# Optimization experiments

Hardware: AMD Instinct MI355X
Metric: run time of the kernel (lower is better)

## Reference

```python
import jax, jax.numpy as jnp
import numpy as np

NUM_HEADS = 32


def setup_inputs() -> dict:
    key = jax.random.key(0)
    ks = jax.random.split(key, 6)
    B, S, E = 1, 2048, 2560
    return {
        "hidden_states": jax.random.normal(ks[0], (B, S, E), dtype=jnp.float32),
        "attention_mask": jnp.zeros((B, 1, 1, S), dtype=jnp.float32),
        "position_bias": jax.random.normal(ks[1], (NUM_HEADS, S, S), dtype=jnp.float32),
        "c_attn_w": jax.random.normal(ks[2], (E, 3 * E), dtype=jnp.float32) * 0.02,
        "c_attn_b": jax.random.normal(ks[3], (3 * E,), dtype=jnp.float32) * 0.02,
        "c_proj_w": jax.random.normal(ks[4], (E, E), dtype=jnp.float32) * 0.02,
        "c_proj_b": jax.random.normal(ks[5], (E,), dtype=jnp.float32) * 0.02,
    }


def reference(hidden_states, attention_mask, position_bias, c_attn_w, c_attn_b, c_proj_w, c_proj_b):
    B, S, E = hidden_states.shape
    H = NUM_HEADS
    D = E // H  # head_dim = 80

    # Fused QKV projection (GPT2-style Conv1D: x @ W + b)
    qkv = hidden_states @ c_attn_w + c_attn_b            # [B, S, 3E]
    q, k, v = jnp.split(qkv, 3, axis=-1)

    def split_heads(t):
        return t.reshape(B, S, H, D).transpose(0, 2, 1, 3)  # [B, H, S, D]

    q, k, v = split_heads(q), split_heads(k), split_heads(v)

    # muP scaling: attn_scale_power=1.0 -> divide by head_dim (not sqrt)
    scores = jnp.einsum("bhqd,bhkd->bhqk", q, k) / jnp.asarray(D, q.dtype)
    scores = scores + attention_mask                     # additive mask [B,1,1,S]
    scores = scores + position_bias[None]                # ALiBi bias [1,H,S,S]

    attn = jax.nn.softmax(scores, axis=-1)               # dropout p=0 -> identity
    out = jnp.einsum("bhqk,bhkd->bhqd", attn, v)         # [B, H, S, D]
    out = out.transpose(0, 2, 1, 3).reshape(B, S, E)     # merge heads

    out = out @ c_proj_w + c_proj_b                      # output projection
    return out
```

## Files before the change

### kernel.cpp

```cpp
#include <hip/hip_runtime.h>
#include <stdint.h>

#define S_LEN 2048
#define EMB   2560
#define NH    32
#define HD    80
#define DP    96

typedef __bf16 bf16x8 __attribute__((ext_vector_type(8)));
typedef float  f32x4  __attribute__((ext_vector_type(4)));

__device__ __forceinline__ ushort f2bf(float x) {
    union { float f; uint32_t u; } v; v.f = x;
    return (ushort)((v.u + 0x7FFFu + ((v.u >> 16) & 1u)) >> 16);
}

__device__ __forceinline__ bf16x8 ldg8(const ushort* p) {
    return *reinterpret_cast<const bf16x8*>(p);
}

__device__ __forceinline__ void gload_lds16(const void* g, void* l) {
    __builtin_amdgcn_global_load_lds((__attribute__((address_space(1))) void*)g,
                                     (__attribute__((address_space(3))) void*)l,
                                     16, 0, 0);
}

__global__ void cvt_f32_bf16(const float* __restrict__ in, ushort* __restrict__ out, int n4) {
    int i = blockIdx.x * blockDim.x + threadIdx.x;
    if (i >= n4) return;
    float4 v = reinterpret_cast<const float4*>(in)[i];
    ushort4 r;
    r.x = f2bf(v.x); r.y = f2bf(v.y); r.z = f2bf(v.z); r.w = f2bf(v.w);
    reinterpret_cast<ushort4*>(out)[i] = r;
}

__global__ void pad_zero(ushort* __restrict__ Qb, ushort* __restrict__ Kb) {
    int i   = blockIdx.x * blockDim.x + threadIdx.x;
    int row = i & 65535;
    ushort* base = ((i >> 16) ? Kb : Qb) + (size_t)row * DP + HD;
    uint4 z = {0, 0, 0, 0};
    *reinterpret_cast<uint4*>(base)     = z;
    *reinterpret_cast<uint4*>(base + 8) = z;
}

__global__ void transpose_cvt(const float* __restrict__ in, ushort* __restrict__ out, int R, int C) {
    __shared__ float tile[32][33];
    const int bx = blockIdx.x << 5;
    const int by = blockIdx.y << 5;
    const int tx = threadIdx.x, ty = threadIdx.y;
#pragma unroll
    for (int i = 0; i < 4; ++i)
        tile[ty + 8 * i][tx] = in[(size_t)(by + ty + 8 * i) * C + bx + tx];
    __syncthreads();
#pragma unroll
    for (int i = 0; i < 4; ++i)
        out[(size_t)(bx + ty + 8 * i) * R + by + tx] = f2bf(tile[tx][ty + 8 * i]);
}

template <int EPI>
__global__ __launch_bounds__(256)
void gemm_bt(const ushort* __restrict__ A, const ushort* __restrict__ BT,
             int M, int N, int Kd, const float* __restrict__ bvec,
             ushort* __restrict__ Qo, ushort* __restrict__ Ko, ushort* __restrict__ Vo,
             float* __restrict__ Co)
{
    __shared__ ushort As[128 * 64];
    __shared__ ushort Bs[128 * 64];

    const int nbn = N >> 7;
    const int nwg = gridDim.x;
    const int cpx = nwg >> 3;
    const int bid = blockIdx.x;
    const int wg  = (bid & 7) * cpx + (bid >> 3);
    const int bm  = wg / nbn;
    const int bn  = wg - bm * nbn;

    const int tid  = threadIdx.x;
    const int w    = tid >> 6, lane = tid & 63;
    const int lo   = lane & 15, hi = lane >> 4;
    const int wr   = w >> 1, wc = w & 1;

    const int srow  = tid >> 3;
    const int sbyte = (tid & 7) << 4;

    f32x4 acc[4][4] = {};

    const char* aG = (const char*)(A  + (size_t)bm * 128 * Kd);
    const char* bG = (const char*)(BT + (size_t)bn * 128 * Kd);
    const size_t rowBytes = (size_t)Kd * 2;

    for (int k0 = 0; k0 < Kd; k0 += 64) {
        __syncthreads();
#pragma unroll
        for (int is = 0; is < 4; ++is) {
            int r  = (is << 5) + srow;
            int sw = sbyte ^ ((r & 7) << 4);
            const char* ga = aG + (size_t)r * rowBytes + (size_t)k0 * 2 + sw;
            const char* gb = bG + (size_t)r * rowBytes + (size_t)k0 * 2 + sw;
            char* la = (char*)As + (is << 12) + (w << 10);
            char* lb = (char*)Bs + (is << 12) + (w << 10);
            gload_lds16(ga, la);
            gload_lds16(gb, lb);
        }
        asm volatile("s_waitcnt vmcnt(0)" ::: "memory");
        __syncthreads();
#pragma unroll
        for (int kk = 0; kk < 2; ++kk) {
            bf16x8 af[4], bf[4];
#pragma unroll
            for (int m = 0; m < 4; ++m) {
                int r   = (wr << 6) + (m << 4) + lo;
                int off = (r << 7) + ((((kk << 6) + (hi << 4))) ^ ((r & 7) << 4));
                af[m] = *(const bf16x8*)((const char*)As + off);
            }
#pragma unroll
            for (int n = 0; n < 4; ++n) {
                int r   = (wc << 6) + (n << 4) + lo;
                int off = (r << 7) + ((((kk << 6) + (hi << 4))) ^ ((r & 7) << 4));
                bf[n] = *(const bf16x8*)((const char*)Bs + off);
            }
#pragma unroll
            for (int m = 0; m < 4; ++m)
#pragma unroll
                for (int n = 0; n < 4; ++n)
                    acc[m][n] = __builtin_amdgcn_mfma_f32_16x16x32_bf16(af[m], bf[n], acc[m][n], 0, 0, 0);
        }
    }

    const int gr_base = bm * 128 + (wr << 6);
    const int gc_base = bn * 128 + (wc << 6);
#pragma unroll
    for (int m = 0; m < 4; ++m) {
        int gr0 = gr_base + (m << 4) + (hi << 2);
#pragma unroll
        for (int n = 0; n < 4; ++n) {
            int gc = gc_base + (n << 4) + lo;
            float bv = bvec[gc];
            if (EPI == 0) {
                int sec = gc / EMB;
                int rr  = gc - sec * EMB;
                int h   = rr / HD;
                int d   = rr - h * HD;
                if (sec == 2) {
                    ushort4 pk;
                    pk.x = f2bf(acc[m][n][0] + bv);
                    pk.y = f2bf(acc[m][n][1] + bv);
                    pk.z = f2bf(acc[m][n][2] + bv);
                    pk.w = f2bf(acc[m][n][3] + bv);
                    *reinterpret_cast<ushort4*>(Vo + ((size_t)h * HD + d) * S_LEN + gr0) = pk;
                } else {
#pragma unroll
                    for (int j = 0; j < 4; ++j) {
                        float vv = acc[m][n][j] + bv;
                        int s = gr0 + j;
                        if (sec == 0) Qo[((size_t)h * S_LEN + s) * DP + d] = f2bf(vv * (1.0f / 80.0f));
                        else          Ko[((size_t)h * S_LEN + s) * DP + d] = f2bf(vv);
                    }
                }
            } else {
#pragma unroll
                for (int j = 0; j < 4; ++j)
                    Co[(size_t)(gr0 + j) * N + gc] = acc[m][n][j] + bv;
            }
        }
    }
}

__global__ __launch_bounds__(512, 4)
void attn_fwd(const ushort* __restrict__ Q, const ushort* __restrict__ K,
              const ushort* __restrict__ VT, const float* __restrict__ bias,
              const float* __restrict__ mask, ushort* __restrict__ ctx)
{
    __shared__ ushort Ks[2][64 * 96];
    __shared__ ushort Vs[2][80 * 64];
    __shared__ ushort P[8][16][72];

    const int bid = blockIdx.x;
    const int l_  = (bid & 7) * 64 + (bid >> 3);
    const int h   = l_ >> 4;
    const int qb  = (l_ & 15) << 7;
    const int tid = threadIdx.x;
    const int w   = tid >> 6, lane = tid & 63;
    const int lo  = lane & 15, hi = lane >> 4;
    const int qrow = qb + (w << 4);

    const ushort* qp = Q + ((size_t)(h * S_LEN + qrow + lo)) * DP + hi * 8;
    bf16x8 qf0 = ldg8(qp), qf1 = ldg8(qp + 32), qf2 = ldg8(qp + 64);

    const char*  kg = (const char*)(K + (size_t)h * S_LEN * DP);
    const char*  vg = (const char*)(VT + (size_t)h * HD * S_LEN);
    const float* bb = bias + (size_t)(h * S_LEN + qrow + hi * 4) * S_LEN + lo;

    int offK0, offK1;
    {
        int b0 = (w << 10) + lane * 16;
        int r0 = b0 / 192, y0 = b0 - r0 * 192;
        offK0 = r0 * 192 + (y0 ^ ((y0 < 128 ? (r0 & 7) : (r0 & 3)) << 4));
        int b1 = ((w + 8) << 10) + lane * 16;
        int r1 = b1 / 192, y1 = b1 - r1 * 192;
        offK1 = r1 * 192 + (y1 ^ ((y1 < 128 ? (r1 & 7) : (r1 & 3)) << 4));
    }

    f32x4 o[5] = {};
    float l_p[4] = {0.f, 0.f, 0.f, 0.f};
    float m_r[4] = {-1e30f, -1e30f, -1e30f, -1e30f};
    float bc[4][4], bn[4][4], mn_[4];

    auto stage_k = [&](int buf, int kt) {
        const char* src = kg + (size_t)kt * 192;
        gload_lds16(src + offK0, (char*)Ks[buf] + (w << 10));
        if (w < 4)
            gload_lds16(src + offK1, (char*)Ks[buf] + ((w + 8) << 10));
    };
    auto stage_v = [&](int buf, int kt) {
        int r0 = (w << 3) + (lane >> 3);
        int s0 = ((lane & 7) << 4) ^ ((r0 & 7) << 4);
        gload_lds16(vg + (size_t)r0 * (S_LEN * 2) + (size_t)kt * 2 + s0,
                    (char*)Vs[buf] + (w << 10));
        if (w < 2) {
            int r1 = ((w + 8) << 3) + (lane >> 3);
            int s1 = ((lane & 7) << 4) ^ ((r1 & 7) << 4);
            gload_lds16(vg + (size_t)r1 * (S_LEN * 2) + (size_t)kt * 2 + s1,
                        (char*)Vs[buf] + ((w + 8) << 10));
        }
    };
    auto bload = [&](int kt) {
#pragma unroll
        for (int n = 0; n < 4; ++n) {
            mn_[n] = mask[kt + n * 16 + lo];
#pragma unroll
            for (int j = 0; j < 4; ++j)
                bn[n][j] = __builtin_nontemporal_load(bb + (size_t)j * S_LEN + kt + n * 16);
        }
    };
    auto rotate = [&]() {
#pragma unroll
        for (int n = 0; n < 4; ++n)
#pragma unroll
            for (int j = 0; j < 4; ++j)
                bc[n][j] = bn[n][j] + mn_[n];
    };

    stage_k(0, 0); stage_v(0, 0); bload(0); rotate();
    __syncthreads();

#pragma unroll 1
    for (int t = 0; t < 32; ++t) {
        const int kt = t << 6;
        const int cb = t & 1;
        if (t < 31) { stage_k(cb ^ 1, kt + 64); stage_v(cb ^ 1, kt + 64); bload(kt + 64); }

        const char* tb = (const char*)Ks[cb];
        f32x4 sc[4] = {};
        __builtin_amdgcn_s_setprio(1);
#pragma unroll
        for (int n = 0; n < 4; ++n) {
            const int r  = (n << 4) + lo;
            const char* rp = tb + r * 192;
            const int s7 = (r & 7) << 4, s3 = (r & 3) << 4;
            sc[n] = __builtin_amdgcn_mfma_f32_16x16x32_bf16(qf0, *(const bf16x8*)(rp + ((hi * 16) ^ s7)),        sc[n], 0, 0, 0);
            sc[n] = __builtin_amdgcn_mfma_f32_16x16x32_bf16(qf1, *(const bf16x8*)(rp + ((64 + hi * 16) ^ s7)),   sc[n], 0, 0, 0);
            sc[n] = __builtin_amdgcn_mfma_f32_16x16x32_bf16(qf2, *(const bf16x8*)(rp + ((128 + hi * 16) ^ s3)),  sc[n], 0, 0, 0);
        }
        __builtin_amdgcn_s_setprio(0);

#pragma unroll
        for (int n = 0; n < 4; ++n)
#pragma unroll
            for (int j = 0; j < 4; ++j)
                sc[n][j] += bc[n][j];

        float tm[4];
#pragma unroll
        for (int j = 0; j < 4; ++j)
            tm[j] = fmaxf(fmaxf(sc[0][j], sc[1][j]), fmaxf(sc[2][j], sc[3][j]));
#pragma unroll
        for (int off = 1; off <= 8; off <<= 1)
#pragma unroll
            for (int j = 0; j < 4; ++j)
                tm[j] = fmaxf(tm[j], __shfl_xor(tm[j], off, 64));

        float al[4];
#pragma unroll
        for (int j = 0; j < 4; ++j) {
            float mnew = fmaxf(m_r[j], tm[j]);
            al[j] = __builtin_amdgcn_exp2f((m_r[j] - mnew) * 1.44269504f);
            m_r[j] = mnew;
            l_p[j] *= al[j];
        }
#pragma unroll
        for (int dn = 0; dn < 5; ++dn)
#pragma unroll
            for (int j = 0; j < 4; ++j)
                o[dn][j] *= al[j];
#pragma unroll
        for (int n = 0; n < 4; ++n)
#pragma unroll
            for (int j = 0; j < 4; ++j) {
                float p = __builtin_amdgcn_exp2f((sc[n][j] - m_r[j]) * 1.44269504f);
                l_p[j] += p;
                P[w][hi * 4 + j][n * 16 + lo] = f2bf(p);
            }
        asm volatile("s_waitcnt lgkmcnt(0)" ::: "memory");
        __builtin_amdgcn_sched_barrier(0);
        bf16x8 pf0 = ldg8(&P[w][lo][hi * 8]);
        bf16x8 pf1 = ldg8(&P[w][lo][32 + hi * 8]);

        const char* vb_ = (const char*)Vs[cb];
        __builtin_amdgcn_s_setprio(1);
#pragma unroll
        for (int dn = 0; dn < 5; ++dn) {
            const int rv = (dn << 4) + lo;
            const char* vp = vb_ + (rv << 7);
            const int sv = (rv & 7) << 4;
            o[dn] = __builtin_amdgcn_mfma_f32_16x16x32_bf16(pf0, *(const bf16x8*)(vp + ((hi * 16) ^ sv)),      o[dn], 0, 0, 0);
            o[dn] = __builtin_amdgcn_mfma_f32_16x16x32_bf16(pf1, *(const bf16x8*)(vp + ((64 + hi * 16) ^ sv)), o[dn], 0, 0, 0);
        }
        __builtin_amdgcn_s_setprio(0);

        rotate();
        __syncthreads();
    }

    float inv[4];
#pragma unroll
    for (int j = 0; j < 4; ++j) {
        float t = l_p[j];
        t += __shfl_xor(t, 1, 64); t += __shfl_xor(t, 2, 64);
        t += __shfl_xor(t, 4, 64); t += __shfl_xor(t, 8, 64);
        inv[j] = 1.0f / t;
    }
    ushort* cp = ctx + (size_t)(qrow + hi * 4) * EMB + h * HD + lo;
#pragma unroll
    for (int dn = 0; dn < 5; ++dn)
#pragma unroll
        for (int j = 0; j < 4; ++j)
            cp[(size_t)j * EMB + dn * 16] = f2bf(o[dn][j] * inv[j]);
}

extern "C" void kernel_launch(void* const* d_in, const int* in_sizes, int n_in,
                              void* d_out, int out_size, void* d_ws, size_t ws_size,
                              hipStream_t stream)
{
    const float* hs     = (const float*)d_in[0];
    const float* mask   = (const float*)d_in[1];
    const float* pbias  = (const float*)d_in[2];
    const float* attn_w = (const float*)d_in[3];
    const float* attn_b = (const float*)d_in[4];
    const float* proj_w = (const float*)d_in[5];
    const float* proj_b = (const float*)d_in[6];
    float* outp = (float*)d_out;

    char* ws = (char*)d_ws;
    ushort* hsB    = (ushort*)(ws);
    ushort* attnWT = (ushort*)(ws + 10485760ull);
    ushort* Qb     = (ushort*)(ws + 49807360ull);
    ushort* Kb     = (ushort*)(ws + 62390272ull);
    ushort* VTb    = (ushort*)(ws + 74973184ull);
    ushort* ctx    = hsB;
    ushort* projWT = attnWT;

    cvt_f32_bf16<<<5120, 256, 0, stream>>>(hs, hsB, 1310720);
    transpose_cvt<<<dim3(7680 / 32, 2560 / 32), dim3(32, 8), 0, stream>>>(attn_w, attnWT, 2560, 7680);
    pad_zero<<<512, 256, 0, stream>>>(Qb, Kb);

    gemm_bt<0><<<960, 256, 0, stream>>>(hsB, attnWT, 2048, 7680, 2560, attn_b,
                                        Qb, Kb, VTb, nullptr);

    attn_fwd<<<512, 512, 0, stream>>>(Qb, Kb, VTb, pbias, mask, ctx);

    transpose_cvt<<<dim3(2560 / 32, 2560 / 32), dim3(32, 8), 0, stream>>>(proj_w, projWT, 2560, 2560);

    gemm_bt<1><<<320, 256, 0, stream>>>(ctx, projWT, 2048, 2560, 2560, proj_b,
                                        nullptr, nullptr, nullptr, outp);
}
```

Baseline: 371.2 us.

## Add 8-wave 128x256 QKV GEMM with triple-buffered direct-to-LDS pipeline

Replaces the generic QKV projection GEMM with a dedicated 512-thread kernel using 128x256 tiles, a three-stage LDS ring filled by global_load_lds with XOR swizzling, and interleaved LDS reads, prefetches and MFMA phases under setprio. The aim is to hide global load latency and raise MFMA utilisation for the largest GEMM. The old template keeps only the output-projection epilogue. The cost is 144 KB of LDS per block, which limits residency to one block per CU, and a hand-scheduled pipeline that is sensitive to the placement of its waitcnt and barrier instructions.

```diff
diff --git a/kernel.cpp b/kernel.cpp
--- a/kernel.cpp
+++ b/kernel.cpp
@@ -55,6 +55,157 @@
 #pragma unroll
     for (int i = 0; i < 4; ++i)
         out[(size_t)(bx + ty + 8 * i) * R + by + tx] = f2bf(tile[tx][ty + 8 * i]);
+}
+
+#define MF(a, b, c) __builtin_amdgcn_mfma_f32_16x16x32_bf16((a), (b), (c), 0, 0, 0)
+
+#define STAGE(kt2, j) do {                                                          \
+    char* _d = Lds + ((kt2) % 3) * 49152 + ldsW[(j)];                               \
+    if ((j) < 2) gload_lds16(aG + (size_t)(kt2) * 128 + srcA[(j)], _d);             \
+    else         gload_lds16(bG + (size_t)(kt2) * 128 + srcB[(j) - 2], _d);         \
+} while (0)
+
+#define LDA(mi, kk) (*(const bf16x8*)(sbase + ((wr * 64 + (mi) * 16 + lo) * 128 +   \
+                      ((((kk) * 64) + hi * 16) ^ ((lo & 7) << 4)))))
+#define LDB(ni, kk) (*(const bf16x8*)(sbase + 16384 +                               \
+                      ((wc * 64 + (ni) * 16 + lo) * 128 +                           \
+                      ((((kk) * 64) + hi * 16) ^ ((lo & 7) << 4)))))
+
+__global__ __launch_bounds__(512)
+void gemm8p_qkv(const ushort* __restrict__ A, const ushort* __restrict__ BT,
+                const float* __restrict__ bvec,
+                ushort* __restrict__ Qo, ushort* __restrict__ Ko, ushort* __restrict__ Vo)
+{
+    __shared__ char Lds[3 * 49152];
+
+    const int NT  = 40;
+    const int nbn = 30;
+    const int bid = blockIdx.x;
+    const int wg  = (bid & 7) * 60 + (bid >> 3);
+    const int bm  = wg / nbn, bn = wg - bm * nbn;
+
+    const int tid = threadIdx.x, w = tid >> 6, lane = tid & 63;
+    const int lo  = lane & 15, hi = lane >> 4;
+    const int wr  = w >> 2, wc = w & 3;
+
+    const char* aG = (const char*)(A  + (size_t)bm * 128 * 2560);
+    const char* bG = (const char*)(BT + (size_t)bn * 256 * 2560);
+
+    int srcA[2], srcB[4], ldsW[6];
+#pragma unroll
+    for (int j = 0; j < 6; ++j) {
+        int Lb = j * 8192 + w * 1024 + lane * 16;
+        ldsW[j] = j * 8192 + w * 1024;
+        int y = Lb & 127;
+        if (j < 2) {
+            int r = Lb >> 7;
+            srcA[j] = r * 5120 + (y ^ ((r & 7) << 4));
+        } else {
+            int r = (Lb - 16384) >> 7;
+            srcB[j - 2] = r * 5120 + (y ^ ((r & 7) << 4));
+        }
+    }
+
+    f32x4  acc[4][4] = {};
+    bf16x8 Afr[2][2], Bfr[4][2];
+
+#pragma unroll
+    for (int j = 0; j < 6; ++j) STAGE(0, j);
+#pragma unroll
+    for (int j = 0; j < 6; ++j) STAGE(1, j);
+
+#pragma unroll 1
+    for (int t = 0; t < NT; ++t) {
+        const char* sbase = Lds + (t % 3) * 49152;
+        const int  t2 = t + 2;
+        const bool pf = (t2 < NT);
+
+        if (t < NT - 1) asm volatile("s_waitcnt vmcnt(6)" ::: "memory");
+        else            asm volatile("s_waitcnt vmcnt(0)" ::: "memory");
+        __builtin_amdgcn_s_barrier();
+
+        Afr[0][0] = LDA(0, 0); Afr[0][1] = LDA(0, 1);
+        Afr[1][0] = LDA(1, 0); Afr[1][1] = LDA(1, 1);
+        Bfr[0][0] = LDB(0, 0); Bfr[0][1] = LDB(0, 1);
+        Bfr[1][0] = LDB(1, 0); Bfr[1][1] = LDB(1, 1);
+        if (pf) { STAGE(t2, 0); STAGE(t2, 1); }
+        __builtin_amdgcn_s_barrier();
+        asm volatile("s_waitcnt lgkmcnt(0)" ::: "memory");
+        __builtin_amdgcn_sched_barrier(0);
+        __builtin_amdgcn_s_setprio(1);
+        acc[0][0] = MF(Afr[0][0], Bfr[0][0], acc[0][0]); acc[0][0] = MF(Afr[0][1], Bfr[0][1], acc[0][0]);
+        acc[0][1] = MF(Afr[0][0], Bfr[1][0], acc[0][1]); acc[0][1] = MF(Afr[0][1], Bfr[1][1], acc[0][1]);
+        acc[1][0] = MF(Afr[1][0], Bfr[0][0], acc[1][0]); acc[1][0] = MF(Afr[1][1], Bfr[0][1], acc[1][0]);
+        acc[1][1] = MF(Afr[1][0], Bfr[1][0], acc[1][1]); acc[1][1] = MF(Afr[1][1], Bfr[1][1], acc[1][1]);
+        __builtin_amdgcn_s_setprio(0);
+
+        Bfr[2][0] = LDB(2, 0); Bfr[2][1] = LDB(2, 1);
+        Bfr[3][0] = LDB(3, 0); Bfr[3][1] = LDB(3, 1);
+        if (pf) { STAGE(t2, 2); STAGE(t2, 3); }
+        __builtin_amdgcn_s_barrier();
+        asm volatile("s_waitcnt lgkmcnt(0)" ::: "memory");
+        __builtin_amdgcn_sched_barrier(0);
+        __builtin_amdgcn_s_setprio(1);
+        acc[0][2] = MF(Afr[0][0], Bfr[2][0], acc[0][2]); acc[0][2] = MF(Afr[0][1], Bfr[2][1], acc[0][2]);
+        acc[0][3] = MF(Afr[0][0], Bfr[3][0], acc[0][3]); acc[0][3] = MF(Afr[0][1], Bfr[3][1], acc[0][3]);
+        acc[1][2] = MF(Afr[1][0], Bfr[2][0], acc[1][2]); acc[1][2] = MF(Afr[1][1], Bfr[2][1], acc[1][2]);
+        acc[1][3] = MF(Afr[1][0], Bfr[3][0], acc[1][3]); acc[1][3] = MF(Afr[1][1], Bfr[3][1], acc[1][3]);
+        __builtin_amdgcn_s_setprio(0);
+
+        Afr[0][0] = LDA(2, 0); Afr[0][1] = LDA(2, 1);
+        Afr[1][0] = LDA(3, 0); Afr[1][1] = LDA(3, 1);
+        if (pf) STAGE(t2, 4);
+        __builtin_amdgcn_s_barrier();
+        asm volatile("s_waitcnt lgkmcnt(0)" ::: "memory");
+        __builtin_amdgcn_sched_barrier(0);
+        __builtin_amdgcn_s_setprio(1);
+        acc[2][2] = MF(Afr[0][0], Bfr[2][0], acc[2][2]); acc[2][2] = MF(Afr[0][1], Bfr[2][1], acc[2][2]);
+        acc[2][3] = MF(Afr[0][0], Bfr[3][0], acc[2][3]); acc[2][3] = MF(Afr[0][1], Bfr[3][1], acc[2][3]);
+        acc[3][2] = MF(Afr[1][0], Bfr[2][0], acc[3][2]); acc[3][2] = MF(Afr[1][1], Bfr[2][1], acc[3][2]);
+        acc[3][3] = MF(Afr[1][0], Bfr[3][0], acc[3][3]); acc[3][3] = MF(Afr[1][1], Bfr[3][1], acc[3][3]);
+        __builtin_amdgcn_s_setprio(0);
+
+        if (pf) STAGE(t2, 5);
+        __builtin_amdgcn_s_barrier();
+        __builtin_amdgcn_s_setprio(1);
+        acc[2][0] = MF(Afr[0][0], Bfr[0][0], acc[2][0]); acc[2][0] = MF(Afr[0][1], Bfr[0][1], acc[2][0]);
+        acc[2][1] = MF(Afr[0][0], Bfr[1][0], acc[2][1]); acc[2][1] = MF(Afr[0][1], Bfr[1][1], acc[2][1]);
+        acc[3][0] = MF(Afr[1][0], Bfr[0][0], acc[3][0]); acc[3][0] = MF(Afr[1][1], Bfr[0][1], acc[3][0]);
+        acc[3][1] = MF(Afr[1][0], Bfr[1][0], acc[3][1]); acc[3][1] = MF(Afr[1][1], Bfr[1][1], acc[3][1]);
+        __builtin_amdgcn_s_setprio(0);
+    }
+
+    const int gr_base = bm * 128 + wr * 64;
+    const int gc_base = bn * 256 + wc * 64;
+#pragma unroll
+    for (int m = 0; m < 4; ++m) {
+        int gr0 = gr_base + (m << 4) + (hi << 2);
+#pragma unroll
+        for (int n = 0; n < 4; ++n) {
+            int gc = gc_base + (n << 4) + lo;
+            float bv = bvec[gc];
+            int sec = gc / EMB;
+            int rr  = gc - sec * EMB;
+            int h   = rr / HD;
+            int d   = rr - h * HD;
+            if (sec == 2) {
+                ushort4 pk;
+                pk.x = f2bf(acc[m][n][0] + bv);
+                pk.y = f2bf(acc[m][n][1] + bv);
+                pk.z = f2bf(acc[m][n][2] + bv);
+                pk.w = f2bf(acc[m][n][3] + bv);
+                *reinterpret_cast<ushort4*>(Vo + ((size_t)h * HD + d) * S_LEN + gr0) = pk;
+            } else {
+#pragma unroll
+                for (int j = 0; j < 4; ++j) {
+                    float vv = acc[m][n][j] + bv;
+                    int s = gr0 + j;
+                    if (sec == 0) Qo[((size_t)h * S_LEN + s) * DP + d] = f2bf(vv * (1.0f / 80.0f));
+                    else          Ko[((size_t)h * S_LEN + s) * DP + d] = f2bf(vv);
+                }
+            }
+        }
+    }
 }
 
 template <int EPI>
@@ -136,32 +287,9 @@
         for (int n = 0; n < 4; ++n) {
             int gc = gc_base + (n << 4) + lo;
             float bv = bvec[gc];
-            if (EPI == 0) {
-                int sec = gc / EMB;
-                int rr  = gc - sec * EMB;
-                int h   = rr / HD;
-                int d   = rr - h * HD;
-                if (sec == 2) {
-                    ushort4 pk;
-                    pk.x = f2bf(acc[m][n][0] + bv);
-                    pk.y = f2bf(acc[m][n][1] + bv);
-                    pk.z = f2bf(acc[m][n][2] + bv);
-                    pk.w = f2bf(acc[m][n][3] + bv);
-                    *reinterpret_cast<ushort4*>(Vo + ((size_t)h * HD + d) * S_LEN + gr0) = pk;
-                } else {
-#pragma unroll
-                    for (int j = 0; j < 4; ++j) {
-                        float vv = acc[m][n][j] + bv;
-                        int s = gr0 + j;
-                        if (sec == 0) Qo[((size_t)h * S_LEN + s) * DP + d] = f2bf(vv * (1.0f / 80.0f));
-                        else          Ko[((size_t)h * S_LEN + s) * DP + d] = f2bf(vv);
-                    }
-                }
-            } else {
-#pragma unroll
-                for (int j = 0; j < 4; ++j)
-                    Co[(size_t)(gr0 + j) * N + gc] = acc[m][n][j] + bv;
-            }
+#pragma unroll
+            for (int j = 0; j < 4; ++j)
+                Co[(size_t)(gr0 + j) * N + gc] = acc[m][n][j] + bv;
         }
     }
 }
@@ -364,8 +492,7 @@
     transpose_cvt<<<dim3(7680 / 32, 2560 / 32), dim3(32, 8), 0, stream>>>(attn_w, attnWT, 2560, 7680);
     pad_zero<<<512, 256, 0, stream>>>(Qb, Kb);
 
-    gemm_bt<0><<<960, 256, 0, stream>>>(hsB, attnWT, 2048, 7680, 2560, attn_b,
-                                        Qb, Kb, VTb, nullptr);
+    gemm8p_qkv<<<480, 512, 0, stream>>>(hsB, attnWT, attn_b, Qb, Kb, VTb);
 
     attn_fwd<<<512, 512, 0, stream>>>(Qb, Kb, VTb, pbias, mask, ctx);
 
```

New measurement: 343.6 us. 1.08x faster.
